# Optimization experiments

Hardware: AMD Instinct MI355X
Metric: run time of the kernel (lower is better)

Reference implementation:

```python
import jax, jax.numpy as jnp
import numpy as np

jax.config.update("jax_enable_x64", True)

N = 256          # nFeatures
B = 64           # batch
C = 10.0         # capacity
DATA_SIZE = 256.0
EPS = 1e-4       # QP regularization strength (Q = EPS * I)
ITERS = 20       # fixed primal-dual interior-point iterations
SIGMA = 0.1      # centering parameter


def build_Gh(indices_male):
    """Constraints for fair_mode=1: sum x <= C, 0 <= x <= 1, fairness band on male subset."""
    m = indices_male.astype(jnp.float64)
    I = jnp.eye(N, dtype=jnp.float64)
    G = jnp.concatenate([jnp.ones((1, N)), -I, I, m[None, :], -m[None, :]], axis=0)  # [2N+3, N]
    rhs_fair = C * m.sum() / DATA_SIZE
    h = jnp.concatenate([
        jnp.array([C]),
        jnp.zeros(N, dtype=jnp.float64),
        jnp.ones(N, dtype=jnp.float64),
        jnp.array([rhs_fair + 1.0]),
        jnp.array([-rhs_fair]),
    ])  # [2N+3]
    return G, h


def solve_qp(p, G, h):
    """Batched PDIPM: min 0.5*EPS*x'x + p'x  s.t. G x <= h.  p: [B, N]."""
    nb, m = p.shape[0], G.shape[0]
    x = jnp.zeros_like(p)
    s = jnp.ones((nb, m), dtype=p.dtype)
    z = jnp.ones((nb, m), dtype=p.dtype)
    I_n = jnp.eye(N, dtype=p.dtype)

    def maxstep(v, dv):
        r = jnp.where(dv < 0, -v / dv, jnp.inf)
        return jnp.min(r, axis=1)

    def step(carry, _):
        x, s, z = carry
        mu = jnp.mean(s * z, axis=1, keepdims=True)
        rx = EPS * x + p + z @ G              # Q x + p + G^T z, [B, N]
        rs = s + x @ G.T - h                  # primal residual (G x + s - h)
        rc = s * z - SIGMA * mu               # complementarity residual
        d = z / s                             # [B, m]
        # Schur complement: Q + G^T diag(d) G, batched over B
        M = EPS * I_n + jnp.einsum('bm,mi,mj->bij', d, G, G)
        rhs = -(rx + ((-rc + z * rs) / s) @ G)
        dx = jnp.linalg.solve(M, rhs[..., None])[..., 0]
        ds = -rs - dx @ G.T
        dz = (-rc - z * ds) / s
        alpha = jnp.minimum(1.0, 0.99 * jnp.minimum(maxstep(s, ds), maxstep(z, dz)))[:, None]
        return (x + alpha * dx, s + alpha * ds, z + alpha * dz), None

    (x, s, z), _ = jax.lax.scan(step, (x, s, z), None, length=ITERS)
    return x


def setup_inputs() -> dict:
    key = jax.random.key(0)
    k1, k2 = jax.random.split(key)
    x = jax.random.normal(k1, (B, N), dtype=jnp.float32)
    indices_male = jax.random.randint(k2, (N,), 0, 2)
    return {"x": x, "indices_male": indices_male}


def reference(x, indices_male):
    G, h = build_Gh(indices_male)
    p = -x.astype(jnp.float64)                # QPFunction(Q, -inputs, ...)
    sol = solve_qp(p, G, h)
    return sol.astype(jnp.float32)
```

## Files before the change

kernel.cpp:

```cpp
#include <hip/hip_runtime.h>
#include <math.h>

#define NF 256
#define NB 64
#define M_CON 515
static constexpr double EPS_Q  = 1e-4;
static constexpr double SIGMA  = 0.1;
static constexpr double CAPC   = 10.0;
static constexpr int    ITERS  = 20;

__device__ __forceinline__ double drcp(double x) {
    double r = __builtin_amdgcn_rcp(x);
    r = fma(r, fma(-x, r, 1.0), r);
    return r;
}
__device__ __forceinline__ double drcp_fast(double x) {
    return __builtin_amdgcn_rcp(x);
}

template <int CTRL>
__device__ __forceinline__ double dpp_d(double v) {
    const int lo = __builtin_amdgcn_update_dpp(0, __double2loint(v), CTRL, 0xF, 0xF, true);
    const int hi = __builtin_amdgcn_update_dpp(0, __double2hiint(v), CTRL, 0xF, 0xF, true);
    return __hiloint2double(hi, lo);
}
__device__ __forceinline__ double bcast63(double v) {
    const int lo = __builtin_amdgcn_readlane(__double2loint(v), 63);
    const int hi = __builtin_amdgcn_readlane(__double2hiint(v), 63);
    return __hiloint2double(hi, lo);
}
__device__ __forceinline__ double wave_red_sum(double v) {
    v += dpp_d<0x121>(v);
    v += dpp_d<0x122>(v);
    v += dpp_d<0x124>(v);
    v += dpp_d<0x128>(v);
    v += dpp_d<0x142>(v);
    v += dpp_d<0x143>(v);
    return bcast63(v);
}
__device__ __forceinline__ double wave_red_max_nn(double v) {
    v = fmax(v, dpp_d<0x121>(v));
    v = fmax(v, dpp_d<0x122>(v));
    v = fmax(v, dpp_d<0x124>(v));
    v = fmax(v, dpp_d<0x128>(v));
    v = fmax(v, dpp_d<0x142>(v));
    v = fmax(v, dpp_d<0x143>(v));
    return bcast63(v);
}

__global__ __launch_bounds__(64)
void pdipm_kernel(const float* __restrict__ xin,
                  const int* __restrict__ male,
                  float* __restrict__ out) {
    const int b = blockIdx.x;
    const int lane = threadIdx.x;

    double e[4], mf[4], x[4];
    double s_lo[4], s_hi[4], z_lo[4], z_hi[4];
    double rs_lo[4], rs_hi[4];
    double msum_p = 0.0;
    #pragma unroll
    for (int k = 0; k < 4; ++k) {
        const int f = lane + 64 * k;
        const double pv = -(double)xin[b * NF + f];
        mf[k] = (double)male[f];
        msum_p += mf[k];
        e[k] = -pv;
        x[k] = 0.0;
        s_lo[k] = 1.0; s_hi[k] = 1.0;
        z_lo[k] = 1.0; z_hi[k] = 1.0;
        rs_lo[k] = 1.0;
        rs_hi[k] = 0.0;
    }
    const double nm = wave_red_sum(msum_p);
    const double rhs_fair = CAPC * nm * (1.0 / 256.0);

    double s0 = 1.0, z0 = 1.0, sA = 1.0, zA = 1.0, sB = 1.0, zB = 1.0;
    double rs0 = 1.0 - CAPC;
    double rsA = -rhs_fair;
    double rsB = 1.0 + rhs_fair;
    double musum = (double)M_CON;

    for (int it = 0; it < ITERS; ++it) {
        const double smu = SIGMA * musum * (1.0 / (double)M_CON);

        const double i_s0 = drcp(s0), i_sA = drcp(sA), i_sB = drcp(sB);
        const double i_z0 = drcp_fast(z0), i_zA = drcp_fast(zA), i_zB = drcp_fast(zB);
        const double d0 = z0 * i_s0, dA = zA * i_sA, dB = zB * i_sB;
        const double beta  = d0 * rs0 + smu * i_s0;
        const double gamma = (dA * rsA + smu * i_sA) - (dB * rsB + smu * i_sB);
        const double ia  = drcp(d0);
        const double ibb = drcp(dA + dB);

        double i_slo[4], i_shi[4], i_zlo[4], i_zhi[4];
        double d_lo[4], d_hi[4], invD[4], y[4];
        double s11_p = 0.0, s12_p = 0.0, t1_p = 0.0, t2_p = 0.0;
        #pragma unroll
        for (int k = 0; k < 4; ++k) {
            i_slo[k] = drcp(s_lo[k]);
            i_shi[k] = drcp(s_hi[k]);
            i_zlo[k] = drcp_fast(z_lo[k]);
            i_zhi[k] = drcp_fast(z_hi[k]);
            d_lo[k] = z_lo[k] * i_slo[k];
            d_hi[k] = z_hi[k] * i_shi[k];
            invD[k] = drcp(EPS_Q + d_lo[k] + d_hi[k]);
            const double rhat = e[k] + d_lo[k] * rs_lo[k] - d_hi[k] * rs_hi[k]
                              + smu * (i_slo[k] - i_shi[k]);
            y[k] = rhat * invD[k];
            s11_p += invD[k];
            s12_p += mf[k] * invD[k];
            t1_p  += y[k];
            t2_p  += mf[k] * y[k];
        }
        const double s11 = wave_red_sum(s11_p);
        const double s12 = wave_red_sum(s12_p);
        const double t1  = wave_red_sum(t1_p);
        const double t2  = wave_red_sum(t2_p);

        const double k11 = ia + s11;
        const double k22 = ibb + s12;
        const double i_det = drcp(k11 * k22 - s12 * s12);
        const double c1 = (k22 * t1 - s12 * t2) * i_det;
        const double c2 = (k11 * t2 - s12 * t1) * i_det;
        const double a1 =  ia * k22 * i_det;
        const double a2 = -ia * s12 * i_det;
        const double b1 = -ibb * s12 * i_det;
        const double b2 =  ibb * k11 * i_det;
        const double C1 = c1 + beta * a1 + gamma * b1;
        const double C2 = c2 + beta * a2 + gamma * b2;
        const double C1pC2 = C1 + C2;

        const double Sdx  = t1 - C1 * s11 - C2 * s12;
        const double Smdx = t2 - C1pC2 * s12;
        const double ds0 = -rs0 - Sdx;
        const double dsA = -rsA - Smdx;
        const double dsB = -rsB + Smdx;
        const double dz0 = smu * i_s0 - z0 - d0 * ds0;
        const double dzA = smu * i_sA - zA - dA * dsA;
        const double dzB = smu * i_sB - zB - dB * dsB;

        double dx[4], ds_lo[4], ds_hi[4], dz_lo[4], dz_hi[4];
        double dsdz_p = 0.0;
        double rmax_p = 0.0;
        #pragma unroll
        for (int k = 0; k < 4; ++k) {
            const double C12 = (mf[k] != 0.0) ? C1pC2 : C1;
            dx[k] = fma(-invD[k], C12, y[k]);
            ds_lo[k] = dx[k] - rs_lo[k];
            ds_hi[k] = -dx[k] - rs_hi[k];
            dz_lo[k] = smu * i_slo[k] - z_lo[k] - d_lo[k] * ds_lo[k];
            dz_hi[k] = smu * i_shi[k] - z_hi[k] - d_hi[k] * ds_hi[k];
            dsdz_p += ds_lo[k] * dz_lo[k] + ds_hi[k] * dz_hi[k];
            const double q1 = -ds_lo[k] * i_slo[k];
            const double q2 = -ds_hi[k] * i_shi[k];
            const double q3 = -dz_lo[k] * i_zlo[k];
            const double q4 = -dz_hi[k] * i_zhi[k];
            rmax_p = fmax(rmax_p, fmax(fmax(q1, q2), fmax(q3, q4)));
        }
        const double Sdsdz_w = wave_red_sum(dsdz_p);
        double rmax = wave_red_max_nn(rmax_p);

        rmax = fmax(rmax, fmax(-ds0 * i_s0, -dz0 * i_z0));
        rmax = fmax(rmax, fmax(-dsA * i_sA, -dzA * i_zA));
        rmax = fmax(rmax, fmax(-dsB * i_sB, -dzB * i_zB));
        const double Sdsdz = Sdsdz_w + ds0 * dz0 + dsA * dzA + dsB * dzB;

        const double alpha = fmin(1.0, 0.99 * drcp_fast(fmax(rmax, 0.99)));
        const double omA = 1.0 - alpha;

        #pragma unroll
        for (int k = 0; k < 4; ++k) {
            const double adx = alpha * dx[k];
            x[k] += adx;
            e[k] = fma(-EPS_Q, adx, e[k]);
            s_lo[k] = fma(alpha, ds_lo[k], s_lo[k]);
            s_hi[k] = fma(alpha, ds_hi[k], s_hi[k]);
            z_lo[k] = fma(alpha, dz_lo[k], z_lo[k]);
            z_hi[k] = fma(alpha, dz_hi[k], z_hi[k]);
            rs_lo[k] *= omA;
            rs_hi[k] *= omA;
        }
        s0 = fma(alpha, ds0, s0); z0 = fma(alpha, dz0, z0);
        sA = fma(alpha, dsA, sA); zA = fma(alpha, dzA, zA);
        sB = fma(alpha, dsB, sB); zB = fma(alpha, dzB, zB);
        rs0 *= omA; rsA *= omA; rsB *= omA;
        musum = musum * (1.0 - alpha * (1.0 - SIGMA)) + alpha * alpha * Sdsdz;
    }

    #pragma unroll
    for (int k = 0; k < 4; ++k)
        out[b * NF + lane + 64 * k] = (float)x[k];
}

extern "C" void kernel_launch(void* const* d_in, const int* in_sizes, int n_in,
                              void* d_out, int out_size, void* d_ws, size_t ws_size,
                              hipStream_t stream) {
    const float* xin  = (const float*)d_in[0];
    const int*   male = (const int*)d_in[1];
    float* out = (float*)d_out;
    pdipm_kernel<<<NB, 64, 0, stream>>>(xin, male, out);
}
```

Before: 72.49 us.

## Process two batch rows per wavefront to interleave independent IPM chains

Each 64-lane block now solves two batch QPs at once, with their per-row state held in registers and every phase interleaved across the two rows. Half as many blocks are launched. The aim is to hide the latency of the serial reductions and reciprocal chains by overlapping two independent dependency chains. The cost is twice the instruction count per wave, more register use, and half as many active CUs. The z reciprocals are also moved to where they are used.

```diff
diff --git a/kernel.cpp b/kernel.cpp
--- a/kernel.cpp
+++ b/kernel.cpp
@@ -48,148 +48,189 @@
     return bcast63(v);
 }
 
-__global__ __launch_bounds__(64)
+__global__ __launch_bounds__(64, 1)
 void pdipm_kernel(const float* __restrict__ xin,
                   const int* __restrict__ male,
                   float* __restrict__ out) {
-    const int b = blockIdx.x;
+    const int b0 = blockIdx.x * 2;
     const int lane = threadIdx.x;
 
-    double e[4], mf[4], x[4];
-    double s_lo[4], s_hi[4], z_lo[4], z_hi[4];
-    double rs_lo[4], rs_hi[4];
+    double mf[4];
+    double e[2][4], x[2][4];
+    double s_lo[2][4], s_hi[2][4], z_lo[2][4], z_hi[2][4];
+    double rs_lo[2][4], rs_hi[2][4];
     double msum_p = 0.0;
     #pragma unroll
     for (int k = 0; k < 4; ++k) {
         const int f = lane + 64 * k;
-        const double pv = -(double)xin[b * NF + f];
         mf[k] = (double)male[f];
         msum_p += mf[k];
-        e[k] = -pv;
-        x[k] = 0.0;
-        s_lo[k] = 1.0; s_hi[k] = 1.0;
-        z_lo[k] = 1.0; z_hi[k] = 1.0;
-        rs_lo[k] = 1.0;
-        rs_hi[k] = 0.0;
+        #pragma unroll
+        for (int i = 0; i < 2; ++i) {
+            const double pv = -(double)xin[(b0 + i) * NF + f];
+            e[i][k] = -pv;
+            x[i][k] = 0.0;
+            s_lo[i][k] = 1.0; s_hi[i][k] = 1.0;
+            z_lo[i][k] = 1.0; z_hi[i][k] = 1.0;
+            rs_lo[i][k] = 1.0;
+            rs_hi[i][k] = 0.0;
+        }
     }
     const double nm = wave_red_sum(msum_p);
     const double rhs_fair = CAPC * nm * (1.0 / 256.0);
 
-    double s0 = 1.0, z0 = 1.0, sA = 1.0, zA = 1.0, sB = 1.0, zB = 1.0;
-    double rs0 = 1.0 - CAPC;
-    double rsA = -rhs_fair;
-    double rsB = 1.0 + rhs_fair;
-    double musum = (double)M_CON;
+    double s0[2], z0[2], sA[2], zA[2], sB[2], zB[2];
+    double rs0[2], rsA[2], rsB[2], musum[2];
+    #pragma unroll
+    for (int i = 0; i < 2; ++i) {
+        s0[i] = 1.0; z0[i] = 1.0; sA[i] = 1.0; zA[i] = 1.0; sB[i] = 1.0; zB[i] = 1.0;
+        rs0[i] = 1.0 - CAPC;
+        rsA[i] = -rhs_fair;
+        rsB[i] = 1.0 + rhs_fair;
+        musum[i] = (double)M_CON;
+    }
 
     for (int it = 0; it < ITERS; ++it) {
-        const double smu = SIGMA * musum * (1.0 / (double)M_CON);
-
-        const double i_s0 = drcp(s0), i_sA = drcp(sA), i_sB = drcp(sB);
-        const double i_z0 = drcp_fast(z0), i_zA = drcp_fast(zA), i_zB = drcp_fast(zB);
-        const double d0 = z0 * i_s0, dA = zA * i_sA, dB = zB * i_sB;
-        const double beta  = d0 * rs0 + smu * i_s0;
-        const double gamma = (dA * rsA + smu * i_sA) - (dB * rsB + smu * i_sB);
-        const double ia  = drcp(d0);
-        const double ibb = drcp(dA + dB);
-
-        double i_slo[4], i_shi[4], i_zlo[4], i_zhi[4];
-        double d_lo[4], d_hi[4], invD[4], y[4];
-        double s11_p = 0.0, s12_p = 0.0, t1_p = 0.0, t2_p = 0.0;
+        double smu[2], i_s0[2], i_sA[2], i_sB[2], i_z0[2], i_zA[2], i_zB[2];
+        double d0[2], dA[2], dB[2], beta[2], gamma[2], ia[2], ibb[2];
+        #pragma unroll
+        for (int i = 0; i < 2; ++i) {
+            smu[i] = SIGMA * musum[i] * (1.0 / (double)M_CON);
+            i_s0[i] = drcp(s0[i]); i_sA[i] = drcp(sA[i]); i_sB[i] = drcp(sB[i]);
+            i_z0[i] = drcp_fast(z0[i]); i_zA[i] = drcp_fast(zA[i]); i_zB[i] = drcp_fast(zB[i]);
+            d0[i] = z0[i] * i_s0[i]; dA[i] = zA[i] * i_sA[i]; dB[i] = zB[i] * i_sB[i];
+            beta[i]  = d0[i] * rs0[i] + smu[i] * i_s0[i];
+            gamma[i] = (dA[i] * rsA[i] + smu[i] * i_sA[i]) - (dB[i] * rsB[i] + smu[i] * i_sB[i]);
+            ia[i]  = drcp(d0[i]);
+            ibb[i] = drcp(dA[i] + dB[i]);
+        }
+
+        double i_slo[2][4], i_shi[2][4];
+        double d_lo[2][4], d_hi[2][4], invD[2][4], y[2][4];
+        double s11_p[2] = {0.0, 0.0}, s12_p[2] = {0.0, 0.0};
+        double t1_p[2]  = {0.0, 0.0}, t2_p[2]  = {0.0, 0.0};
         #pragma unroll
         for (int k = 0; k < 4; ++k) {
-            i_slo[k] = drcp(s_lo[k]);
-            i_shi[k] = drcp(s_hi[k]);
-            i_zlo[k] = drcp_fast(z_lo[k]);
-            i_zhi[k] = drcp_fast(z_hi[k]);
-            d_lo[k] = z_lo[k] * i_slo[k];
-            d_hi[k] = z_hi[k] * i_shi[k];
-            invD[k] = drcp(EPS_Q + d_lo[k] + d_hi[k]);
-            const double rhat = e[k] + d_lo[k] * rs_lo[k] - d_hi[k] * rs_hi[k]
-                              + smu * (i_slo[k] - i_shi[k]);
-            y[k] = rhat * invD[k];
-            s11_p += invD[k];
-            s12_p += mf[k] * invD[k];
-            t1_p  += y[k];
-            t2_p  += mf[k] * y[k];
-        }
-        const double s11 = wave_red_sum(s11_p);
-        const double s12 = wave_red_sum(s12_p);
-        const double t1  = wave_red_sum(t1_p);
-        const double t2  = wave_red_sum(t2_p);
-
-        const double k11 = ia + s11;
-        const double k22 = ibb + s12;
-        const double i_det = drcp(k11 * k22 - s12 * s12);
-        const double c1 = (k22 * t1 - s12 * t2) * i_det;
-        const double c2 = (k11 * t2 - s12 * t1) * i_det;
-        const double a1 =  ia * k22 * i_det;
-        const double a2 = -ia * s12 * i_det;
-        const double b1 = -ibb * s12 * i_det;
-        const double b2 =  ibb * k11 * i_det;
-        const double C1 = c1 + beta * a1 + gamma * b1;
-        const double C2 = c2 + beta * a2 + gamma * b2;
-        const double C1pC2 = C1 + C2;
-
-        const double Sdx  = t1 - C1 * s11 - C2 * s12;
-        const double Smdx = t2 - C1pC2 * s12;
-        const double ds0 = -rs0 - Sdx;
-        const double dsA = -rsA - Smdx;
-        const double dsB = -rsB + Smdx;
-        const double dz0 = smu * i_s0 - z0 - d0 * ds0;
-        const double dzA = smu * i_sA - zA - dA * dsA;
-        const double dzB = smu * i_sB - zB - dB * dsB;
-
-        double dx[4], ds_lo[4], ds_hi[4], dz_lo[4], dz_hi[4];
-        double dsdz_p = 0.0;
-        double rmax_p = 0.0;
+            #pragma unroll
+            for (int i = 0; i < 2; ++i) {
+                i_slo[i][k] = drcp(s_lo[i][k]);
+                i_shi[i][k] = drcp(s_hi[i][k]);
+                d_lo[i][k] = z_lo[i][k] * i_slo[i][k];
+                d_hi[i][k] = z_hi[i][k] * i_shi[i][k];
+                invD[i][k] = drcp(EPS_Q + d_lo[i][k] + d_hi[i][k]);
+                const double rhat = e[i][k] + d_lo[i][k] * rs_lo[i][k] - d_hi[i][k] * rs_hi[i][k]
+                                  + smu[i] * (i_slo[i][k] - i_shi[i][k]);
+                y[i][k] = rhat * invD[i][k];
+                s11_p[i] += invD[i][k];
+                s12_p[i] += mf[k] * invD[i][k];
+                t1_p[i]  += y[i][k];
+                t2_p[i]  += mf[k] * y[i][k];
+            }
+        }
+        double s11[2], s12[2], t1[2], t2[2];
+        #pragma unroll
+        for (int i = 0; i < 2; ++i) {
+            s11[i] = wave_red_sum(s11_p[i]);
+            s12[i] = wave_red_sum(s12_p[i]);
+            t1[i]  = wave_red_sum(t1_p[i]);
+            t2[i]  = wave_red_sum(t2_p[i]);
+        }
+
+        double C1[2], C2[2], C1pC2[2];
+        double ds0[2], dsA[2], dsB[2], dz0[2], dzA[2], dzB[2];
+        #pragma unroll
+        for (int i = 0; i < 2; ++i) {
+            const double k11 = ia[i] + s11[i];
+            const double k22 = ibb[i] + s12[i];
+            const double i_det = drcp(k11 * k22 - s12[i] * s12[i]);
+            const double c1 = (k22 * t1[i] - s12[i] * t2[i]) * i_det;
+            const double c2 = (k11 * t2[i] - s12[i] * t1[i]) * i_det;
+            const double a1 =  ia[i] * k22 * i_det;
+            const double a2 = -ia[i] * s12[i] * i_det;
+            const double b1 = -ibb[i] * s12[i] * i_det;
+            const double b2 =  ibb[i] * k11 * i_det;
+            C1[i] = c1 + beta[i] * a1 + gamma[i] * b1;
+            C2[i] = c2 + beta[i] * a2 + gamma[i] * b2;
+            C1pC2[i] = C1[i] + C2[i];
+
+            const double Sdx  = t1[i] - C1[i] * s11[i] - C2[i] * s12[i];
+            const double Smdx = t2[i] - C1pC2[i] * s12[i];
+            ds0[i] = -rs0[i] - Sdx;
+            dsA[i] = -rsA[i] - Smdx;
+            dsB[i] = -rsB[i] + Smdx;
+            dz0[i] = smu[i] * i_s0[i] - z0[i] - d0[i] * ds0[i];
+            dzA[i] = smu[i] * i_sA[i] - zA[i] - dA[i] * dsA[i];
+            dzB[i] = smu[i] * i_sB[i] - zB[i] - dB[i] * dsB[i];
+        }
+
+        double dx[2][4], ds_lo[2][4], ds_hi[2][4], dz_lo[2][4], dz_hi[2][4];
+        double dsdz_p[2] = {0.0, 0.0};
+        double rmax_p[2] = {0.0, 0.0};
         #pragma unroll
         for (int k = 0; k < 4; ++k) {
-            const double C12 = (mf[k] != 0.0) ? C1pC2 : C1;
-            dx[k] = fma(-invD[k], C12, y[k]);
-            ds_lo[k] = dx[k] - rs_lo[k];
-            ds_hi[k] = -dx[k] - rs_hi[k];
-            dz_lo[k] = smu * i_slo[k] - z_lo[k] - d_lo[k] * ds_lo[k];
-            dz_hi[k] = smu * i_shi[k] - z_hi[k] - d_hi[k] * ds_hi[k];
-            dsdz_p += ds_lo[k] * dz_lo[k] + ds_hi[k] * dz_hi[k];
-            const double q1 = -ds_lo[k] * i_slo[k];
-            const double q2 = -ds_hi[k] * i_shi[k];
-            const double q3 = -dz_lo[k] * i_zlo[k];
-            const double q4 = -dz_hi[k] * i_zhi[k];
-            rmax_p = fmax(rmax_p, fmax(fmax(q1, q2), fmax(q3, q4)));
-        }
-        const double Sdsdz_w = wave_red_sum(dsdz_p);
-        double rmax = wave_red_max_nn(rmax_p);
-
-        rmax = fmax(rmax, fmax(-ds0 * i_s0, -dz0 * i_z0));
-        rmax = fmax(rmax, fmax(-dsA * i_sA, -dzA * i_zA));
-        rmax = fmax(rmax, fmax(-dsB * i_sB, -dzB * i_zB));
-        const double Sdsdz = Sdsdz_w + ds0 * dz0 + dsA * dzA + dsB * dzB;
-
-        const double alpha = fmin(1.0, 0.99 * drcp_fast(fmax(rmax, 0.99)));
-        const double omA = 1.0 - alpha;
+            #pragma unroll
+            for (int i = 0; i < 2; ++i) {
+                const double C12 = (mf[k] != 0.0) ? C1pC2[i] : C1[i];
+                dx[i][k] = fma(-invD[i][k], C12, y[i][k]);
+                ds_lo[i][k] = dx[i][k] - rs_lo[i][k];
+                ds_hi[i][k] = -dx[i][k] - rs_hi[i][k];
+                dz_lo[i][k] = smu[i] * i_slo[i][k] - z_lo[i][k] - d_lo[i][k] * ds_lo[i][k];
+                dz_hi[i][k] = smu[i] * i_shi[i][k] - z_hi[i][k] - d_hi[i][k] * ds_hi[i][k];
+                dsdz_p[i] += ds_lo[i][k] * dz_lo[i][k] + ds_hi[i][k] * dz_hi[i][k];
+                const double i_zlo = drcp_fast(z_lo[i][k]);
+                const double i_zhi = drcp_fast(z_hi[i][k]);
+                const double q1 = -ds_lo[i][k] * i_slo[i][k];
+                const double q2 = -ds_hi[i][k] * i_shi[i][k];
+                const double q3 = -dz_lo[i][k] * i_zlo;
+                const double q4 = -dz_hi[i][k] * i_zhi;
+                rmax_p[i] = fmax(rmax_p[i], fmax(fmax(q1, q2), fmax(q3, q4)));
+            }
+        }
+
+        double Sdsdz[2], alpha[2], omA[2];
+        #pragma unroll
+        for (int i = 0; i < 2; ++i) {
+            const double Sdsdz_w = wave_red_sum(dsdz_p[i]);
+            double rmax = wave_red_max_nn(rmax_p[i]);
+            rmax = fmax(rmax, fmax(-ds0[i] * i_s0[i], -dz0[i] * i_z0[i]));
+            rmax = fmax(rmax, fmax(-dsA[i] * i_sA[i], -dzA[i] * i_zA[i]));
+            rmax = fmax(rmax, fmax(-dsB[i] * i_sB[i], -dzB[i] * i_zB[i]));
+            Sdsdz[i] = Sdsdz_w + ds0[i] * dz0[i] + dsA[i] * dzA[i] + dsB[i] * dzB[i];
+            alpha[i] = fmin(1.0, 0.99 * drcp_fast(fmax(rmax, 0.99)));
+            omA[i] = 1.0 - alpha[i];
+        }
 
         #pragma unroll
         for (int k = 0; k < 4; ++k) {
-            const double adx = alpha * dx[k];
-            x[k] += adx;
-            e[k] = fma(-EPS_Q, adx, e[k]);
-            s_lo[k] = fma(alpha, ds_lo[k], s_lo[k]);
-            s_hi[k] = fma(alpha, ds_hi[k], s_hi[k]);
-            z_lo[k] = fma(alpha, dz_lo[k], z_lo[k]);
-            z_hi[k] = fma(alpha, dz_hi[k], z_hi[k]);
-            rs_lo[k] *= omA;
-            rs_hi[k] *= omA;
-        }
-        s0 = fma(alpha, ds0, s0); z0 = fma(alpha, dz0, z0);
-        sA = fma(alpha, dsA, sA); zA = fma(alpha, dzA, zA);
-        sB = fma(alpha, dsB, sB); zB = fma(alpha, dzB, zB);
-        rs0 *= omA; rsA *= omA; rsB *= omA;
-        musum = musum * (1.0 - alpha * (1.0 - SIGMA)) + alpha * alpha * Sdsdz;
+            #pragma unroll
+            for (int i = 0; i < 2; ++i) {
+                const double adx = alpha[i] * dx[i][k];
+                x[i][k] += adx;
+                e[i][k] = fma(-EPS_Q, adx, e[i][k]);
+                s_lo[i][k] = fma(alpha[i], ds_lo[i][k], s_lo[i][k]);
+                s_hi[i][k] = fma(alpha[i], ds_hi[i][k], s_hi[i][k]);
+                z_lo[i][k] = fma(alpha[i], dz_lo[i][k], z_lo[i][k]);
+                z_hi[i][k] = fma(alpha[i], dz_hi[i][k], z_hi[i][k]);
+                rs_lo[i][k] *= omA[i];
+                rs_hi[i][k] *= omA[i];
+            }
+        }
+        #pragma unroll
+        for (int i = 0; i < 2; ++i) {
+            s0[i] = fma(alpha[i], ds0[i], s0[i]); z0[i] = fma(alpha[i], dz0[i], z0[i]);
+            sA[i] = fma(alpha[i], dsA[i], sA[i]); zA[i] = fma(alpha[i], dzA[i], zA[i]);
+            sB[i] = fma(alpha[i], dsB[i], sB[i]); zB[i] = fma(alpha[i], dzB[i], zB[i]);
+            rs0[i] *= omA[i]; rsA[i] *= omA[i]; rsB[i] *= omA[i];
+            musum[i] = musum[i] * (1.0 - alpha[i] * (1.0 - SIGMA))
+                     + alpha[i] * alpha[i] * Sdsdz[i];
+        }
     }
 
     #pragma unroll
     for (int k = 0; k < 4; ++k)
-        out[b * NF + lane + 64 * k] = (float)x[k];
+        #pragma unroll
+        for (int i = 0; i < 2; ++i)
+            out[(b0 + i) * NF + lane + 64 * k] = (float)x[i][k];
 }
 
 extern "C" void kernel_launch(void* const* d_in, const int* in_sizes, int n_in,
@@ -198,5 +239,5 @@
     const float* xin  = (const float*)d_in[0];
     const int*   male = (const int*)d_in[1];
     float* out = (float*)d_out;
-    pdipm_kernel<<<NB, 64, 0, stream>>>(xin, male, out);
-}
+    pdipm_kernel<<<NB / 2, 64, 0, stream>>>(xin, male, out);
+}
```

Result: slower. 98.71 us (+36.2%).

## Spread each batch row across four waves with shared-memory cross-wave reductions

Applied to the files above, without the earlier changes.

Each batch row is now handled by a 256-thread block with one feature per thread, instead of a single 64-lane wave processing four features per lane. Wave-level DPP reductions now leave their partials in lane 63, which writes them to small shared arrays; after a barrier every thread combines the four wave partials. The always-zero upper-bound residual is dropped. This cuts the serial per-wave instruction stream by spreading the fp64 work over four waves, at the cost of two block barriers and LDS round trips per iteration.

```diff
diff --git a/kernel.cpp b/kernel.cpp
--- a/kernel.cpp
+++ b/kernel.cpp
@@ -24,55 +24,50 @@
     const int hi = __builtin_amdgcn_update_dpp(0, __double2hiint(v), CTRL, 0xF, 0xF, true);
     return __hiloint2double(hi, lo);
 }
-__device__ __forceinline__ double bcast63(double v) {
-    const int lo = __builtin_amdgcn_readlane(__double2loint(v), 63);
-    const int hi = __builtin_amdgcn_readlane(__double2hiint(v), 63);
-    return __hiloint2double(hi, lo);
-}
-__device__ __forceinline__ double wave_red_sum(double v) {
+__device__ __forceinline__ double wave_sum_l63(double v) {
     v += dpp_d<0x121>(v);
     v += dpp_d<0x122>(v);
     v += dpp_d<0x124>(v);
     v += dpp_d<0x128>(v);
     v += dpp_d<0x142>(v);
     v += dpp_d<0x143>(v);
-    return bcast63(v);
+    return v;
 }
-__device__ __forceinline__ double wave_red_max_nn(double v) {
+__device__ __forceinline__ double wave_max_nn_l63(double v) {
     v = fmax(v, dpp_d<0x121>(v));
     v = fmax(v, dpp_d<0x122>(v));
     v = fmax(v, dpp_d<0x124>(v));
     v = fmax(v, dpp_d<0x128>(v));
     v = fmax(v, dpp_d<0x142>(v));
     v = fmax(v, dpp_d<0x143>(v));
-    return bcast63(v);
+    return v;
 }
 
-__global__ __launch_bounds__(64)
+__global__ __launch_bounds__(256, 1)
 void pdipm_kernel(const float* __restrict__ xin,
                   const int* __restrict__ male,
                   float* __restrict__ out) {
     const int b = blockIdx.x;
-    const int lane = threadIdx.x;
+    const int tid = threadIdx.x;
+    const int lane = tid & 63;
+    const int w = tid >> 6;
 
-    double e[4], mf[4], x[4];
-    double s_lo[4], s_hi[4], z_lo[4], z_hi[4];
-    double rs_lo[4], rs_hi[4];
-    double msum_p = 0.0;
-    #pragma unroll
-    for (int k = 0; k < 4; ++k) {
-        const int f = lane + 64 * k;
-        const double pv = -(double)xin[b * NF + f];
-        mf[k] = (double)male[f];
-        msum_p += mf[k];
-        e[k] = -pv;
-        x[k] = 0.0;
-        s_lo[k] = 1.0; s_hi[k] = 1.0;
-        z_lo[k] = 1.0; z_hi[k] = 1.0;
-        rs_lo[k] = 1.0;
-        rs_hi[k] = 0.0;
+    __shared__ double red1[4][4];
+    __shared__ double red2[2][4];
+
+    const double mf = (double)male[tid];
+    double e = (double)xin[b * NF + tid];
+    double x = 0.0;
+    double s_lo = 1.0, s_hi = 1.0, z_lo = 1.0, z_hi = 1.0;
+    double rs_l = 1.0;
+
+    {
+        const double v = wave_sum_l63(mf);
+        if (lane == 63) red1[0][w] = v;
     }
-    const double nm = wave_red_sum(msum_p);
+    __syncthreads();
+    const double nm = (red1[0][0] + red1[0][1]) + (red1[0][2] + red1[0][3]);
+    __syncthreads();
     const double rhs_fair = CAPC * nm * (1.0 / 256.0);
 
     double s0 = 1.0, z0 = 1.0, sA = 1.0, zA = 1.0, sB = 1.0, zB = 1.0;
@@ -92,30 +87,26 @@
         const double ia  = drcp(d0);
         const double ibb = drcp(dA + dB);
 
-        double i_slo[4], i_shi[4], i_zlo[4], i_zhi[4];
-        double d_lo[4], d_hi[4], invD[4], y[4];
-        double s11_p = 0.0, s12_p = 0.0, t1_p = 0.0, t2_p = 0.0;
-        #pragma unroll
-        for (int k = 0; k < 4; ++k) {
-            i_slo[k] = drcp(s_lo[k]);
-            i_shi[k] = drcp(s_hi[k]);
-            i_zlo[k] = drcp_fast(z_lo[k]);
-            i_zhi[k] = drcp_fast(z_hi[k]);
-            d_lo[k] = z_lo[k] * i_slo[k];
-            d_hi[k] = z_hi[k] * i_shi[k];
-            invD[k] = drcp(EPS_Q + d_lo[k] + d_hi[k]);
-            const double rhat = e[k] + d_lo[k] * rs_lo[k] - d_hi[k] * rs_hi[k]
-                              + smu * (i_slo[k] - i_shi[k]);
-            y[k] = rhat * invD[k];
-            s11_p += invD[k];
-            s12_p += mf[k] * invD[k];
-            t1_p  += y[k];
-            t2_p  += mf[k] * y[k];
+        const double i_slo = drcp(s_lo);
+        const double i_shi = drcp(s_hi);
+        const double d_lo = z_lo * i_slo;
+        const double d_hi = z_hi * i_shi;
+        const double invD = drcp(EPS_Q + d_lo + d_hi);
+        const double rhat = e + d_lo * rs_l + smu * (i_slo - i_shi);
+        const double y = rhat * invD;
+
+        const double p0 = wave_sum_l63(invD);
+        const double p1 = wave_sum_l63(mf * invD);
+        const double p2 = wave_sum_l63(y);
+        const double p3 = wave_sum_l63(mf * y);
+        if (lane == 63) {
+            red1[0][w] = p0; red1[1][w] = p1; red1[2][w] = p2; red1[3][w] = p3;
         }
-        const double s11 = wave_red_sum(s11_p);
-        const double s12 = wave_red_sum(s12_p);
-        const double t1  = wave_red_sum(t1_p);
-        const double t2  = wave_red_sum(t2_p);
+        __syncthreads();
+        const double s11 = (red1[0][0] + red1[0][1]) + (red1[0][2] + red1[0][3]);
+        const double s12 = (red1[1][0] + red1[1][1]) + (red1[1][2] + red1[1][3]);
+        const double t1  = (red1[2][0] + red1[2][1]) + (red1[2][2] + red1[2][3]);
+        const double t2  = (red1[3][0] + red1[3][1]) + (red1[3][2] + red1[3][3]);
 
         const double k11 = ia + s11;
         const double k22 = ibb + s12;
@@ -139,26 +130,28 @@
         const double dzA = smu * i_sA - zA - dA * dsA;
         const double dzB = smu * i_sB - zB - dB * dsB;
 
-        double dx[4], ds_lo[4], ds_hi[4], dz_lo[4], dz_hi[4];
-        double dsdz_p = 0.0;
-        double rmax_p = 0.0;
-        #pragma unroll
-        for (int k = 0; k < 4; ++k) {
-            const double C12 = (mf[k] != 0.0) ? C1pC2 : C1;
-            dx[k] = fma(-invD[k], C12, y[k]);
-            ds_lo[k] = dx[k] - rs_lo[k];
-            ds_hi[k] = -dx[k] - rs_hi[k];
-            dz_lo[k] = smu * i_slo[k] - z_lo[k] - d_lo[k] * ds_lo[k];
-            dz_hi[k] = smu * i_shi[k] - z_hi[k] - d_hi[k] * ds_hi[k];
-            dsdz_p += ds_lo[k] * dz_lo[k] + ds_hi[k] * dz_hi[k];
-            const double q1 = -ds_lo[k] * i_slo[k];
-            const double q2 = -ds_hi[k] * i_shi[k];
-            const double q3 = -dz_lo[k] * i_zlo[k];
-            const double q4 = -dz_hi[k] * i_zhi[k];
-            rmax_p = fmax(rmax_p, fmax(fmax(q1, q2), fmax(q3, q4)));
-        }
-        const double Sdsdz_w = wave_red_sum(dsdz_p);
-        double rmax = wave_red_max_nn(rmax_p);
+        const double C12 = (mf != 0.0) ? C1pC2 : C1;
+        const double dx = fma(-invD, C12, y);
+        const double ds_lo = dx - rs_l;
+        const double ds_hi = -dx;
+        const double dz_lo = smu * i_slo - z_lo - d_lo * ds_lo;
+        const double dz_hi = smu * i_shi - z_hi - d_hi * ds_hi;
+        const double dsdz_p = ds_lo * dz_lo + ds_hi * dz_hi;
+        const double i_zlo = drcp_fast(z_lo);
+        const double i_zhi = drcp_fast(z_hi);
+        const double q1 = -ds_lo * i_slo;
+        const double q2 = -ds_hi * i_shi;
+        const double q3 = -dz_lo * i_zlo;
+        const double q4 = -dz_hi * i_zhi;
+        const double rmax_p = fmax(0.0, fmax(fmax(q1, q2), fmax(q3, q4)));
+
+        const double pp0 = wave_sum_l63(dsdz_p);
+        const double pp1 = wave_max_nn_l63(rmax_p);
+        if (lane == 63) { red2[0][w] = pp0; red2[1][w] = pp1; }
+        __syncthreads();
+        const double Sdsdz_w = (red2[0][0] + red2[0][1]) + (red2[0][2] + red2[0][3]);
+        double rmax = fmax(fmax(red2[1][0], red2[1][1]),
+                           fmax(red2[1][2], red2[1][3]));
 
         rmax = fmax(rmax, fmax(-ds0 * i_s0, -dz0 * i_z0));
         rmax = fmax(rmax, fmax(-dsA * i_sA, -dzA * i_zA));
@@ -168,18 +161,15 @@
         const double alpha = fmin(1.0, 0.99 * drcp_fast(fmax(rmax, 0.99)));
         const double omA = 1.0 - alpha;
 
-        #pragma unroll
-        for (int k = 0; k < 4; ++k) {
-            const double adx = alpha * dx[k];
-            x[k] += adx;
-            e[k] = fma(-EPS_Q, adx, e[k]);
-            s_lo[k] = fma(alpha, ds_lo[k], s_lo[k]);
-            s_hi[k] = fma(alpha, ds_hi[k], s_hi[k]);
-            z_lo[k] = fma(alpha, dz_lo[k], z_lo[k]);
-            z_hi[k] = fma(alpha, dz_hi[k], z_hi[k]);
-            rs_lo[k] *= omA;
-            rs_hi[k] *= omA;
-        }
+        const double adx = alpha * dx;
+        x += adx;
+        e = fma(-EPS_Q, adx, e);
+        s_lo = fma(alpha, ds_lo, s_lo);
+        s_hi = fma(alpha, ds_hi, s_hi);
+        z_lo = fma(alpha, dz_lo, z_lo);
+        z_hi = fma(alpha, dz_hi, z_hi);
+        rs_l *= omA;
+
         s0 = fma(alpha, ds0, s0); z0 = fma(alpha, dz0, z0);
         sA = fma(alpha, dsA, sA); zA = fma(alpha, dzA, zA);
         sB = fma(alpha, dsB, sB); zB = fma(alpha, dzB, zB);
@@ -187,9 +177,7 @@
         musum = musum * (1.0 - alpha * (1.0 - SIGMA)) + alpha * alpha * Sdsdz;
     }
 
-    #pragma unroll
-    for (int k = 0; k < 4; ++k)
-        out[b * NF + lane + 64 * k] = (float)x[k];
+    out[b * NF + tid] = (float)x;
 }
 
 extern "C" void kernel_launch(void* const* d_in, const int* in_sizes, int n_in,
@@ -198,5 +186,5 @@
     const float* xin  = (const float*)d_in[0];
     const int*   male = (const int*)d_in[1];
     float* out = (float*)d_out;
-    pdipm_kernel<<<NB, 64, 0, stream>>>(xin, male, out);
+    pdipm_kernel<<<NB, 256, 0, stream>>>(xin, male, out);
 }
```

After: 72.46 us. Within noise of the previous version (-0.0%).
